# Kernel optimization log

Measured on AMD Instinct MI355X. Metric: run time of the kernel, lower is better.

The kernel has to match this reference:

```python
import jax, jax.numpy as jnp
import numpy as np

D_MODEL = 1024

def setup_inputs() -> dict:
    key = jax.random.key(0)
    ks = jax.random.split(key, 7)
    x = jax.random.normal(ks[0], (4, 2048, D_MODEL), dtype=jnp.float32)
    s = 1.0 / np.sqrt(D_MODEL)
    Wq = jax.random.uniform(ks[1], (D_MODEL, D_MODEL), jnp.float32, -s, s)
    bq = jax.random.uniform(ks[2], (D_MODEL,), jnp.float32, -s, s)
    Wk = jax.random.uniform(ks[3], (D_MODEL, D_MODEL), jnp.float32, -s, s)
    bk = jax.random.uniform(ks[4], (D_MODEL,), jnp.float32, -s, s)
    Wv = jax.random.uniform(ks[5], (D_MODEL, D_MODEL), jnp.float32, -s, s)
    bv = jax.random.uniform(ks[6], (D_MODEL,), jnp.float32, -s, s)
    return {"x": x, "Wq": Wq, "bq": bq, "Wk": Wk, "bk": bk, "Wv": Wv, "bv": bv}

def reference(x, Wq, bq, Wk, bk, Wv, bv):
    # single-head self-attention: q,k,v are [B, S, D]
    q = x @ Wq + bq
    k = x @ Wk + bk
    v = x @ Wv + bv
    scale = 1.0 / jnp.sqrt(jnp.asarray(D_MODEL, x.dtype))
    scores = jnp.einsum('bsd,btd->bst', q, k) * scale  # [B, S, S]
    attn = jax.nn.softmax(scores, axis=-1)
    return jnp.einsum('bst,btd->bsd', attn, v)
```

## Files before the change

kernel.cpp:

```cpp
#include <hip/hip_runtime.h>
#include <hip/hip_bf16.h>
#include <stdint.h>


typedef __attribute__((ext_vector_type(8))) short short8;
typedef __attribute__((ext_vector_type(4))) float f32x4;

__device__ __forceinline__ unsigned short f2bf(float f) {
  union { float f; uint32_t u; } c; c.f = f;
  uint32_t u = c.u;
  u += 0x7FFFu + ((u >> 16) & 1u);
  return (unsigned short)(u >> 16);
}

__device__ __forceinline__ void gl16(const void* g, void* l) {
  __builtin_amdgcn_global_load_lds(
      (const __attribute__((address_space(1))) unsigned int*)g,
      (__attribute__((address_space(3))) unsigned int*)l, 16, 0, 0);
}

template <int MODE>
__device__ __forceinline__ void gemm_body(
    int z, int tm, int tn,
    const short* __restrict__ A, const short* __restrict__ B,
    void* __restrict__ Cv, short* __restrict__ vT, float scale,
    const float* __restrict__ bias0, const float* __restrict__ bias1,
    const float* __restrict__ bias2, float* __restrict__ rowsum)
{
  constexpr int  LDA = (MODE == 2) ? 2048 : 1024;
  constexpr int  LDB = (MODE == 2) ? 2048 : 1024;
  constexpr int  LDC = (MODE == 0) ? 1024 : ((MODE == 1) ? 2048 : 1024);
  constexpr long SAZ = (MODE == 0) ? 0L : ((MODE == 1) ? 2097152L : 4194304L);
  constexpr long SBZ = (MODE == 0) ? 1048576L : 2097152L;
  constexpr long SCZ = (MODE == 0) ? 8388608L : ((MODE == 1) ? 4194304L : 2097152L);
  constexpr int  T   = (MODE == 2) ? 64 : 32;

  __shared__ short lds[18432];

  const int tid  = threadIdx.x;
  const int lane = tid & 63;
  const int wid  = tid >> 6;
  const long tileM = (long)tm * 128;
  const long tileN = (long)tn * 128;
  const short* Az = A + (long)z * SAZ;
  const short* Bz = B + (long)z * SBZ;

  const int c0 = tid, c1 = 256 + tid;
  const short* gA0 = Az + (tileM + (c0 >> 2)) * LDA + (c0 & 3) * 8;
  const short* gA1 = Az + (tileM + (c1 >> 2)) * LDA + (c1 & 3) * 8;
  const short* gB0 = Bz + (tileN + (c0 >> 2)) * LDB + (c0 & 3) * 8;
  const short* gB1 = Bz + (tileN + (c1 >> 2)) * LDB + (c1 & 3) * 8;

  const int fr = lane & 15, quad = lane >> 4;
  const int waveM = (wid >> 1) * 64, waveN = (wid & 1) * 64;

  f32x4 acc[4][4] = {};

  {
    short* base = lds;
    gl16(gA0, base + c0 * 8);
    gl16(gA1, base + c1 * 8);
    gl16(gB0, base + 4096 + c0 * 8);
    gl16(gB1, base + 4096 + c1 * 8);
  }

  for (int t = 0; t < T; ++t) {
    __syncthreads();
    if (t + 1 < T) {
      const int kt = (t + 1) << 5;
      short* base = lds + ((t + 1) & 1) * 8192;
      gl16(gA0 + kt, base + c0 * 8);
      gl16(gA1 + kt, base + c1 * 8);
      gl16(gB0 + kt, base + 4096 + c0 * 8);
      gl16(gB1 + kt, base + 4096 + c1 * 8);
    }
    const short* sA = lds + (t & 1) * 8192;
    const short* sB = sA + 4096;
    short8 af[4], bf[4];
#pragma unroll
    for (int i = 0; i < 4; ++i)
      af[i] = *(const short8*)&sA[(waveM + i * 16 + fr) * 32 + quad * 8];
#pragma unroll
    for (int j = 0; j < 4; ++j)
      bf[j] = *(const short8*)&sB[(waveN + j * 16 + fr) * 32 + quad * 8];
#pragma unroll
    for (int i = 0; i < 4; ++i)
#pragma unroll
      for (int j = 0; j < 4; ++j)
        acc[i][j] = __builtin_amdgcn_mfma_f32_16x16x32_bf16(af[i], bf[j],
                                                            acc[i][j], 0, 0, 0);
  }

  if (MODE == 1) {
#pragma unroll
    for (int i = 0; i < 4; ++i)
#pragma unroll
      for (int j = 0; j < 4; ++j)
#pragma unroll
        for (int r = 0; r < 4; ++r)
          acc[i][j][r] = exp2f(acc[i][j][r] * scale);
#pragma unroll
    for (int i = 0; i < 4; ++i)
#pragma unroll
      for (int r = 0; r < 4; ++r) {
        float s = acc[i][0][r] + acc[i][1][r] + acc[i][2][r] + acc[i][3][r];
        s += __shfl_xor(s, 1);
        s += __shfl_xor(s, 2);
        s += __shfl_xor(s, 4);
        s += __shfl_xor(s, 8);
        if (fr == 0)
          atomicAdd(&rowsum[(long)z * 2048 + tileM + waveM + i * 16 + quad * 4 + r], s);
      }
  }

  if (MODE == 0 && z == 2) {
    __syncthreads();
    short* scr = lds + wid * 4608;
#pragma unroll
    for (int j = 0; j < 4; ++j) {
      const float bv = bias2[tileN + waveN + j * 16 + fr];
#pragma unroll
      for (int i = 0; i < 4; ++i)
#pragma unroll
        for (int r = 0; r < 4; ++r)
          scr[(j * 16 + fr) * 72 + i * 16 + quad * 4 + r] =
              (short)f2bf(acc[i][j][r] + bv);
    }
    const int gb = tm >> 4;
    const long t0 = (long)(tm & 15) * 128 + waveM;
#pragma unroll
    for (int c = 0; c < 8; ++c) {
      const int rr = c * 8 + (lane >> 3);
      const int cc = (lane & 7) * 8;
      short8 v = *(const short8*)&scr[rr * 72 + cc];
      const long gd = tileN + waveN + rr;
      *(short8*)(vT + ((long)gb << 21) + gd * 2048 + t0 + cc) = v;
    }
  } else if (MODE <= 1) {
    __syncthreads();
    short* scr = lds + wid * 4608;
    short* C = (short*)Cv + (long)z * SCZ;
    const float* bias = (z == 0) ? bias0 : bias1;
#pragma unroll
    for (int j = 0; j < 4; ++j) {
      const float bv = (MODE == 0) ? bias[tileN + waveN + j * 16 + fr] : 0.0f;
#pragma unroll
      for (int i = 0; i < 4; ++i)
#pragma unroll
        for (int r = 0; r < 4; ++r)
          scr[(i * 16 + quad * 4 + r) * 72 + j * 16 + fr] =
              (short)f2bf(acc[i][j][r] + bv);
    }
#pragma unroll
    for (int c = 0; c < 8; ++c) {
      const int row = c * 8 + (lane >> 3);
      const int col = (lane & 7) * 8;
      short8 v = *(const short8*)&scr[row * 72 + col];
      *(short8*)(C + (tileM + waveM + row) * LDC + tileN + waveN + col) = v;
    }
  } else {
    float* C = (float*)Cv + (long)z * SCZ;
#pragma unroll
    for (int i = 0; i < 4; ++i)
#pragma unroll
      for (int r = 0; r < 4; ++r) {
        const long gr = tileM + waveM + i * 16 + quad * 4 + r;
        const float rinv = 1.0f / rowsum[(long)z * 2048 + gr];
#pragma unroll
        for (int j = 0; j < 4; ++j)
          C[gr * LDC + tileN + waveN + j * 16 + fr] = acc[i][j][r] * rinv;
      }
  }
}

__global__ __launch_bounds__(256) void k_qkv(
    const short* __restrict__ A, const short* __restrict__ B,
    void* __restrict__ Cv, short* __restrict__ vT,
    const float* __restrict__ b0, const float* __restrict__ b1,
    const float* __restrict__ b2)
{
  gemm_body<0>(blockIdx.z, blockIdx.y, blockIdx.x, A, B, Cv, vT, 1.0f,
               b0, b1, b2, nullptr);
}

__global__ __launch_bounds__(256) void k_score(
    const short* __restrict__ A, const short* __restrict__ B,
    void* __restrict__ Cv, float scale, float* __restrict__ rowsum)
{
  const int b = blockIdx.x;
  const int xcd = b & 7, r = b >> 3;
  const int z = r >> 5;
  const int pair = (r >> 4) & 1, mem = r & 15;
  const int s = pair * 8 + xcd;
  const int tm = (s >> 2) * 4 + (mem >> 2);
  const int tn = (s & 3) * 4 + (mem & 3);
  gemm_body<1>(z, tm, tn, A, B, Cv, nullptr, scale,
               nullptr, nullptr, nullptr, rowsum);
}

__global__ __launch_bounds__(256) void k_pv(
    const short* __restrict__ A, const short* __restrict__ B,
    void* __restrict__ Cv, float* __restrict__ rowsum)
{
  const int b = blockIdx.x;
  const int s = b & 7, r = b >> 3;
  const int z = r >> 4;
  const int mem = r & 15;
  const int tm = (s >> 1) * 4 + (mem >> 2);
  const int tn = (s & 1) * 4 + (mem & 3);
  gemm_body<2>(z, tm, tn, A, B, Cv, nullptr, 1.0f,
               nullptr, nullptr, nullptr, rowsum);
}

__global__ __launch_bounds__(256) void k_prep(
    const float4* __restrict__ x, ushort4* __restrict__ xb,
    const float* __restrict__ Wq, const float* __restrict__ Wk,
    const float* __restrict__ Wv, short* __restrict__ WT,
    float* __restrict__ rs)
{
  __shared__ short tile[32][33];
  const int b = blockIdx.x;
  if (b < 8192) {
    const long i = (long)b * 256 + threadIdx.x;
    float4 v = x[i];
    ushort4 o;
    o.x = f2bf(v.x); o.y = f2bf(v.y); o.z = f2bf(v.z); o.w = f2bf(v.w);
    xb[i] = o;
  } else if (b < 11264) {
    const int idx = b - 8192;
    const int z = idx >> 10, rem = idx & 1023;
    const float* W = (z == 0) ? Wq : ((z == 1) ? Wk : Wv);
    short* d = WT + (long)z * 1024 * 1024;
    const int n0 = (rem & 31) * 32, d0 = (rem >> 5) * 32;
    const int tx = threadIdx.x & 31, ty = threadIdx.x >> 5;
#pragma unroll
    for (int p = 0; p < 4; ++p)
      tile[ty + p * 8][tx] = (short)f2bf(W[(long)(d0 + ty + p * 8) * 1024 + n0 + tx]);
    __syncthreads();
#pragma unroll
    for (int p = 0; p < 4; ++p)
      d[(long)(n0 + ty + p * 8) * 1024 + d0 + tx] = tile[tx][ty + p * 8];
  } else {
#pragma unroll
    for (int p = 0; p < 32; ++p)
      rs[p * 256 + threadIdx.x] = 0.0f;
  }
}

extern "C" void kernel_launch(void* const* d_in, const int* in_sizes, int n_in,
                              void* d_out, int out_size, void* d_ws, size_t ws_size,
                              hipStream_t stream) {
  const float* x  = (const float*)d_in[0];
  const float* Wq = (const float*)d_in[1];
  const float* bq = (const float*)d_in[2];
  const float* Wk = (const float*)d_in[3];
  const float* bk = (const float*)d_in[4];
  const float* Wv = (const float*)d_in[5];
  const float* bv = (const float*)d_in[6];

  char* ws = (char*)d_ws;
  short* xb  = (short*)(ws);
  short* wt  = (short*)(ws + 16777216);
  short* qkv = (short*)(ws + 23068672);
  short* Pp  = (short*)(ws + 73400320);
  float* rs  = (float*)(ws + 106954752);
  short* vT  = qkv + 2L * 8388608;

  k_prep<<<11265, 256, 0, stream>>>((const float4*)x, (ushort4*)xb,
                                    Wq, Wk, Wv, wt, rs);
  k_qkv<<<dim3(8, 64, 3), 256, 0, stream>>>(xb, wt, qkv, vT, bq, bk, bv);
  k_score<<<1024, 256, 0, stream>>>(qkv, qkv + 8388608, Pp,
                                    0.03125f * 1.44269504088896f, rs);
  k_pv<<<512, 256, 0, stream>>>(Pp, vT, d_out, rs);
}
```

Measured before the change: 279.1 us.

## Use 64x128 tiles with 128-thread blocks for score and PV GEMMs

Splits the shared GEMM template so the QKV projection keeps 128x128 tiles, while the score and PV GEMMs use 64x128 tiles with two waves per block. This doubles their grid sizes and changes the tile-to-block mapping, dropping the XCD-aware ordering. The V transpose moves out of the QKV epilogue into a separate LDS-tiled transpose kernel with its own workspace buffer. The smaller tiles aim for better occupancy and load balance, at the cost of less reuse per block, an extra kernel launch and an extra pass over V in global memory.

Result: slower. 313.6 us (+12.3%).

```diff
diff --git a/kernel.cpp b/kernel.cpp
--- a/kernel.cpp
+++ b/kernel.cpp
@@ -19,37 +19,28 @@
       (__attribute__((address_space(3))) unsigned int*)l, 16, 0, 0);
 }
 
-template <int MODE>
-__device__ __forceinline__ void gemm_body(
-    int z, int tm, int tn,
+__global__ __launch_bounds__(256) void k_qkv(
     const short* __restrict__ A, const short* __restrict__ B,
-    void* __restrict__ Cv, short* __restrict__ vT, float scale,
-    const float* __restrict__ bias0, const float* __restrict__ bias1,
-    const float* __restrict__ bias2, float* __restrict__ rowsum)
-{
-  constexpr int  LDA = (MODE == 2) ? 2048 : 1024;
-  constexpr int  LDB = (MODE == 2) ? 2048 : 1024;
-  constexpr int  LDC = (MODE == 0) ? 1024 : ((MODE == 1) ? 2048 : 1024);
-  constexpr long SAZ = (MODE == 0) ? 0L : ((MODE == 1) ? 2097152L : 4194304L);
-  constexpr long SBZ = (MODE == 0) ? 1048576L : 2097152L;
-  constexpr long SCZ = (MODE == 0) ? 8388608L : ((MODE == 1) ? 4194304L : 2097152L);
-  constexpr int  T   = (MODE == 2) ? 64 : 32;
-
+    short* __restrict__ Cb,
+    const float* __restrict__ b0, const float* __restrict__ b1,
+    const float* __restrict__ b2)
+{
   __shared__ short lds[18432];
 
   const int tid  = threadIdx.x;
   const int lane = tid & 63;
   const int wid  = tid >> 6;
-  const long tileM = (long)tm * 128;
-  const long tileN = (long)tn * 128;
-  const short* Az = A + (long)z * SAZ;
-  const short* Bz = B + (long)z * SBZ;
+  const int z    = blockIdx.z;
+  const long tileM = (long)blockIdx.y * 128;
+  const long tileN = (long)blockIdx.x * 128;
+  const short* Az = A;
+  const short* Bz = B + (long)z * 1048576L;
 
   const int c0 = tid, c1 = 256 + tid;
-  const short* gA0 = Az + (tileM + (c0 >> 2)) * LDA + (c0 & 3) * 8;
-  const short* gA1 = Az + (tileM + (c1 >> 2)) * LDA + (c1 & 3) * 8;
-  const short* gB0 = Bz + (tileN + (c0 >> 2)) * LDB + (c0 & 3) * 8;
-  const short* gB1 = Bz + (tileN + (c1 >> 2)) * LDB + (c1 & 3) * 8;
+  const short* gA0 = Az + (tileM + (c0 >> 2)) * 1024 + (c0 & 3) * 8;
+  const short* gA1 = Az + (tileM + (c1 >> 2)) * 1024 + (c1 & 3) * 8;
+  const short* gB0 = Bz + (tileN + (c0 >> 2)) * 1024 + (c0 & 3) * 8;
+  const short* gB1 = Bz + (tileN + (c1 >> 2)) * 1024 + (c1 & 3) * 8;
 
   const int fr = lane & 15, quad = lane >> 4;
   const int waveM = (wid >> 1) * 64, waveN = (wid & 1) * 64;
@@ -64,9 +55,9 @@
     gl16(gB1, base + 4096 + c1 * 8);
   }
 
-  for (int t = 0; t < T; ++t) {
+  for (int t = 0; t < 32; ++t) {
     __syncthreads();
-    if (t + 1 < T) {
+    if (t + 1 < 32) {
       const int kt = (t + 1) << 5;
       short* base = lds + ((t + 1) & 1) * 8192;
       gl16(gA0 + kt, base + c0 * 8);
@@ -91,6 +82,106 @@
                                                             acc[i][j], 0, 0, 0);
   }
 
+  __syncthreads();
+  short* scr = lds + wid * 4608;
+  short* C = Cb + (long)z * 8388608L;
+  const float* bias = (z == 0) ? b0 : ((z == 1) ? b1 : b2);
+#pragma unroll
+  for (int j = 0; j < 4; ++j) {
+    const float bv = bias[tileN + waveN + j * 16 + fr];
+#pragma unroll
+    for (int i = 0; i < 4; ++i)
+#pragma unroll
+      for (int r = 0; r < 4; ++r)
+        scr[(i * 16 + quad * 4 + r) * 72 + j * 16 + fr] =
+            (short)f2bf(acc[i][j][r] + bv);
+  }
+#pragma unroll
+  for (int c = 0; c < 8; ++c) {
+    const int row = c * 8 + (lane >> 3);
+    const int col = (lane & 7) * 8;
+    short8 v = *(const short8*)&scr[row * 72 + col];
+    *(short8*)(C + (tileM + waveM + row) * 1024 + tileN + waveN + col) = v;
+  }
+}
+
+template <int MODE>
+__device__ __forceinline__ void body128(
+    int z, int tm, int tn,
+    const short* __restrict__ A, const short* __restrict__ B,
+    void* __restrict__ Cv, float scale, float* __restrict__ rowsum)
+{
+  constexpr int  LDA = (MODE == 2) ? 2048 : 1024;
+  constexpr int  LDB = (MODE == 2) ? 2048 : 1024;
+  constexpr int  LDC = (MODE == 1) ? 2048 : 1024;
+  constexpr long SAZ = (MODE == 1) ? 2097152L : 4194304L;
+  constexpr long SBZ = 2097152L;
+  constexpr long SCZ = (MODE == 1) ? 4194304L : 2097152L;
+  constexpr int  T   = (MODE == 2) ? 64 : 32;
+
+  __shared__ short lds[12288];
+
+  const int tid  = threadIdx.x;
+  const int lane = tid & 63;
+  const int wid  = tid >> 6;
+  const long tileM = (long)tm * 64;
+  const long tileN = (long)tn * 128;
+  const short* Az = A + (long)z * SAZ;
+  const short* Bz = B + (long)z * SBZ;
+
+  const int cA0 = tid, cA1 = 128 + tid;
+  const short* gA0 = Az + (tileM + (cA0 >> 2)) * LDA + (cA0 & 3) * 8;
+  const short* gA1 = Az + (tileM + (cA1 >> 2)) * LDA + (cA1 & 3) * 8;
+  const int cB0 = tid, cB1 = 128 + tid, cB2 = 256 + tid, cB3 = 384 + tid;
+  const short* gB0 = Bz + (tileN + (cB0 >> 2)) * LDB + (cB0 & 3) * 8;
+  const short* gB1 = Bz + (tileN + (cB1 >> 2)) * LDB + (cB1 & 3) * 8;
+  const short* gB2 = Bz + (tileN + (cB2 >> 2)) * LDB + (cB2 & 3) * 8;
+  const short* gB3 = Bz + (tileN + (cB3 >> 2)) * LDB + (cB3 & 3) * 8;
+
+  const int fr = lane & 15, quad = lane >> 4;
+  const int waveN = wid * 64;
+
+  f32x4 acc[4][4] = {};
+
+  {
+    short* base = lds;
+    gl16(gA0, base + cA0 * 8);
+    gl16(gA1, base + cA1 * 8);
+    gl16(gB0, base + 2048 + cB0 * 8);
+    gl16(gB1, base + 2048 + cB1 * 8);
+    gl16(gB2, base + 2048 + cB2 * 8);
+    gl16(gB3, base + 2048 + cB3 * 8);
+  }
+
+  for (int t = 0; t < T; ++t) {
+    __syncthreads();
+    if (t + 1 < T) {
+      const int kt = (t + 1) << 5;
+      short* base = lds + ((t + 1) & 1) * 6144;
+      gl16(gA0 + kt, base + cA0 * 8);
+      gl16(gA1 + kt, base + cA1 * 8);
+      gl16(gB0 + kt, base + 2048 + cB0 * 8);
+      gl16(gB1 + kt, base + 2048 + cB1 * 8);
+      gl16(gB2 + kt, base + 2048 + cB2 * 8);
+      gl16(gB3 + kt, base + 2048 + cB3 * 8);
+    }
+    const short* sA = lds + (t & 1) * 6144;
+    const short* sB = sA + 2048;
+    short8 af[4], bf[4];
+#pragma unroll
+    for (int i = 0; i < 4; ++i)
+      af[i] = *(const short8*)&sA[(i * 16 + fr) * 32 + quad * 8];
+#pragma unroll
+    for (int j = 0; j < 4; ++j)
+      bf[j] = *(const short8*)&sB[(waveN + j * 16 + fr) * 32 + quad * 8];
+#pragma unroll
+    for (int i = 0; i < 4; ++i)
+#pragma unroll
+      for (int j = 0; j < 4; ++j)
+        acc[i][j] = __builtin_amdgcn_mfma_f32_16x16x32_bf16(af[i], bf[j],
+                                                            acc[i][j], 0, 0, 0);
+  }
+
   if (MODE == 1) {
 #pragma unroll
     for (int i = 0; i < 4; ++i)
@@ -109,54 +200,25 @@
         s += __shfl_xor(s, 4);
         s += __shfl_xor(s, 8);
         if (fr == 0)
-          atomicAdd(&rowsum[(long)z * 2048 + tileM + waveM + i * 16 + quad * 4 + r], s);
+          atomicAdd(&rowsum[(long)z * 2048 + tileM + i * 16 + quad * 4 + r], s);
       }
-  }
-
-  if (MODE == 0 && z == 2) {
-    __syncthreads();
-    short* scr = lds + wid * 4608;
-#pragma unroll
-    for (int j = 0; j < 4; ++j) {
-      const float bv = bias2[tileN + waveN + j * 16 + fr];
-#pragma unroll
-      for (int i = 0; i < 4; ++i)
-#pragma unroll
-        for (int r = 0; r < 4; ++r)
-          scr[(j * 16 + fr) * 72 + i * 16 + quad * 4 + r] =
-              (short)f2bf(acc[i][j][r] + bv);
-    }
-    const int gb = tm >> 4;
-    const long t0 = (long)(tm & 15) * 128 + waveM;
-#pragma unroll
-    for (int c = 0; c < 8; ++c) {
-      const int rr = c * 8 + (lane >> 3);
-      const int cc = (lane & 7) * 8;
-      short8 v = *(const short8*)&scr[rr * 72 + cc];
-      const long gd = tileN + waveN + rr;
-      *(short8*)(vT + ((long)gb << 21) + gd * 2048 + t0 + cc) = v;
-    }
-  } else if (MODE <= 1) {
     __syncthreads();
     short* scr = lds + wid * 4608;
     short* C = (short*)Cv + (long)z * SCZ;
-    const float* bias = (z == 0) ? bias0 : bias1;
-#pragma unroll
-    for (int j = 0; j < 4; ++j) {
-      const float bv = (MODE == 0) ? bias[tileN + waveN + j * 16 + fr] : 0.0f;
+#pragma unroll
+    for (int j = 0; j < 4; ++j)
 #pragma unroll
       for (int i = 0; i < 4; ++i)
 #pragma unroll
         for (int r = 0; r < 4; ++r)
           scr[(i * 16 + quad * 4 + r) * 72 + j * 16 + fr] =
-              (short)f2bf(acc[i][j][r] + bv);
-    }
+              (short)f2bf(acc[i][j][r]);
 #pragma unroll
     for (int c = 0; c < 8; ++c) {
       const int row = c * 8 + (lane >> 3);
       const int col = (lane & 7) * 8;
       short8 v = *(const short8*)&scr[row * 72 + col];
-      *(short8*)(C + (tileM + waveM + row) * LDC + tileN + waveN + col) = v;
+      *(short8*)(C + (tileM + row) * LDC + tileN + waveN + col) = v;
     }
   } else {
     float* C = (float*)Cv + (long)z * SCZ;
@@ -164,7 +226,7 @@
     for (int i = 0; i < 4; ++i)
 #pragma unroll
       for (int r = 0; r < 4; ++r) {
-        const long gr = tileM + waveM + i * 16 + quad * 4 + r;
+        const long gr = tileM + i * 16 + quad * 4 + r;
         const float rinv = 1.0f / rowsum[(long)z * 2048 + gr];
 #pragma unroll
         for (int j = 0; j < 4; ++j)
@@ -173,43 +235,46 @@
   }
 }
 
-__global__ __launch_bounds__(256) void k_qkv(
-    const short* __restrict__ A, const short* __restrict__ B,
-    void* __restrict__ Cv, short* __restrict__ vT,
-    const float* __restrict__ b0, const float* __restrict__ b1,
-    const float* __restrict__ b2)
-{
-  gemm_body<0>(blockIdx.z, blockIdx.y, blockIdx.x, A, B, Cv, vT, 1.0f,
-               b0, b1, b2, nullptr);
-}
-
-__global__ __launch_bounds__(256) void k_score(
+__global__ __launch_bounds__(128) void k_score(
     const short* __restrict__ A, const short* __restrict__ B,
     void* __restrict__ Cv, float scale, float* __restrict__ rowsum)
 {
   const int b = blockIdx.x;
-  const int xcd = b & 7, r = b >> 3;
-  const int z = r >> 5;
-  const int pair = (r >> 4) & 1, mem = r & 15;
-  const int s = pair * 8 + xcd;
-  const int tm = (s >> 2) * 4 + (mem >> 2);
-  const int tn = (s & 3) * 4 + (mem & 3);
-  gemm_body<1>(z, tm, tn, A, B, Cv, nullptr, scale,
-               nullptr, nullptr, nullptr, rowsum);
-}
-
-__global__ __launch_bounds__(256) void k_pv(
+  const int z = b >> 9, rest = b & 511;
+  const int super = rest >> 4, inner = rest & 15;
+  const int tm = (super >> 2) * 4 + (inner >> 2);
+  const int tn = (super & 3) * 4 + (inner & 3);
+  body128<1>(z, tm, tn, A, B, Cv, scale, rowsum);
+}
+
+__global__ __launch_bounds__(128) void k_pv(
     const short* __restrict__ A, const short* __restrict__ B,
     void* __restrict__ Cv, float* __restrict__ rowsum)
 {
   const int b = blockIdx.x;
-  const int s = b & 7, r = b >> 3;
-  const int z = r >> 4;
-  const int mem = r & 15;
-  const int tm = (s >> 1) * 4 + (mem >> 2);
-  const int tn = (s & 1) * 4 + (mem & 3);
-  gemm_body<2>(z, tm, tn, A, B, Cv, nullptr, 1.0f,
-               nullptr, nullptr, nullptr, rowsum);
+  const int z = b >> 8, rest = b & 255;
+  const int super = rest >> 4, inner = rest & 15;
+  const int tm = (super >> 1) * 4 + (inner >> 2);
+  const int tn = (super & 1) * 4 + (inner & 3);
+  body128<2>(z, tm, tn, A, B, Cv, 1.0f, rowsum);
+}
+
+__global__ __launch_bounds__(256) void k_tr(
+    const short* __restrict__ src, short* __restrict__ dst)
+{
+  __shared__ short tile[32][33];
+  const int z = blockIdx.z;
+  const int d0 = blockIdx.x * 32, t0 = blockIdx.y * 32;
+  const int tx = threadIdx.x & 31, ty = threadIdx.x >> 5;
+  const short* s = src + (long)z * 2048 * 1024;
+  short* d = dst + (long)z * 1024 * 2048;
+#pragma unroll
+  for (int p = 0; p < 4; ++p)
+    tile[ty + p * 8][tx] = s[(long)(t0 + ty + p * 8) * 1024 + d0 + tx];
+  __syncthreads();
+#pragma unroll
+  for (int p = 0; p < 4; ++p)
+    d[(long)(d0 + ty + p * 8) * 2048 + t0 + tx] = tile[tx][ty + p * 8];
 }
 
 __global__ __launch_bounds__(256) void k_prep(
@@ -264,12 +329,13 @@
   short* qkv = (short*)(ws + 23068672);
   short* Pp  = (short*)(ws + 73400320);
   float* rs  = (float*)(ws + 106954752);
-  short* vT  = qkv + 2L * 8388608;
+  short* vT  = (short*)(ws + 106987520);
 
   k_prep<<<11265, 256, 0, stream>>>((const float4*)x, (ushort4*)xb,
                                     Wq, Wk, Wv, wt, rs);
-  k_qkv<<<dim3(8, 64, 3), 256, 0, stream>>>(xb, wt, qkv, vT, bq, bk, bv);
-  k_score<<<1024, 256, 0, stream>>>(qkv, qkv + 8388608, Pp,
+  k_qkv<<<dim3(8, 64, 3), 256, 0, stream>>>(xb, wt, qkv, bq, bk, bv);
+  k_tr<<<dim3(32, 64, 4), 256, 0, stream>>>(qkv + 2L * 8388608, vT);
+  k_score<<<2048, 128, 0, stream>>>(qkv, qkv + 8388608, Pp,
                                     0.03125f * 1.44269504088896f, rs);
-  k_pv<<<512, 256, 0, stream>>>(Pp, vT, d_out, rs);
-}
+  k_pv<<<1024, 128, 0, stream>>>(Pp, vT, d_out, rs);
+}
```

## Use 256x256 tiles with 1024-thread blocks for scores and XCD-aware QKV grid mapping

Applied to the files above, without the earlier changes.

The templated GEMM body is split into three specialized kernels. The score GEMM now uses 256x256 output tiles with 16 waves per 1024-thread block, and each block loads the whole K tile for the larger tile. That raises operand reuse and halves global loads per output element. The QKV kernel gets a 1D grid remapped so that the M-tiles sharing one XCD are grouped together, aiming at better L2 locality. The trade-off is larger LDS use, lower occupancy, and a serialized four-round epilogue for writing the score tiles.

Result: faster. 256.2 us (-8.2%).

```diff
diff --git a/kernel.cpp b/kernel.cpp
--- a/kernel.cpp
+++ b/kernel.cpp
@@ -19,21 +19,18 @@
       (__attribute__((address_space(3))) unsigned int*)l, 16, 0, 0);
 }
 
-template <int MODE>
-__device__ __forceinline__ void gemm_body(
-    int z, int tm, int tn,
+__global__ __launch_bounds__(256) void k_qkv(
     const short* __restrict__ A, const short* __restrict__ B,
-    void* __restrict__ Cv, short* __restrict__ vT, float scale,
-    const float* __restrict__ bias0, const float* __restrict__ bias1,
-    const float* __restrict__ bias2, float* __restrict__ rowsum)
+    short* __restrict__ Cb, short* __restrict__ vT,
+    const float* __restrict__ b0, const float* __restrict__ b1,
+    const float* __restrict__ b2)
 {
-  constexpr int  LDA = (MODE == 2) ? 2048 : 1024;
-  constexpr int  LDB = (MODE == 2) ? 2048 : 1024;
-  constexpr int  LDC = (MODE == 0) ? 1024 : ((MODE == 1) ? 2048 : 1024);
-  constexpr long SAZ = (MODE == 0) ? 0L : ((MODE == 1) ? 2097152L : 4194304L);
-  constexpr long SBZ = (MODE == 0) ? 1048576L : 2097152L;
-  constexpr long SCZ = (MODE == 0) ? 8388608L : ((MODE == 1) ? 4194304L : 2097152L);
-  constexpr int  T   = (MODE == 2) ? 64 : 32;
+  const int b = blockIdx.x;
+  const int xcd = b & 7, r = b >> 3;
+  const int z = r >> 6;
+  const int mem = r & 63;
+  const int tm = xcd * 8 + (mem >> 3);
+  const int tn = mem & 7;
 
   __shared__ short lds[18432];
 
@@ -42,14 +39,14 @@
   const int wid  = tid >> 6;
   const long tileM = (long)tm * 128;
   const long tileN = (long)tn * 128;
-  const short* Az = A + (long)z * SAZ;
-  const short* Bz = B + (long)z * SBZ;
+  const short* Az = A;
+  const short* Bz = B + (long)z * 1048576L;
 
   const int c0 = tid, c1 = 256 + tid;
-  const short* gA0 = Az + (tileM + (c0 >> 2)) * LDA + (c0 & 3) * 8;
-  const short* gA1 = Az + (tileM + (c1 >> 2)) * LDA + (c1 & 3) * 8;
-  const short* gB0 = Bz + (tileN + (c0 >> 2)) * LDB + (c0 & 3) * 8;
-  const short* gB1 = Bz + (tileN + (c1 >> 2)) * LDB + (c1 & 3) * 8;
+  const short* gA0 = Az + (tileM + (c0 >> 2)) * 1024 + (c0 & 3) * 8;
+  const short* gA1 = Az + (tileM + (c1 >> 2)) * 1024 + (c1 & 3) * 8;
+  const short* gB0 = Bz + (tileN + (c0 >> 2)) * 1024 + (c0 & 3) * 8;
+  const short* gB1 = Bz + (tileN + (c1 >> 2)) * 1024 + (c1 & 3) * 8;
 
   const int fr = lane & 15, quad = lane >> 4;
   const int waveM = (wid >> 1) * 64, waveN = (wid & 1) * 64;
@@ -64,9 +61,9 @@
     gl16(gB1, base + 4096 + c1 * 8);
   }
 
-  for (int t = 0; t < T; ++t) {
-    __syncthreads();
-    if (t + 1 < T) {
+  for (int t = 0; t < 32; ++t) {
+    __syncthreads();
+    if (t + 1 < 32) {
       const int kt = (t + 1) << 5;
       short* base = lds + ((t + 1) & 1) * 8192;
       gl16(gA0 + kt, base + c0 * 8);
@@ -91,34 +88,12 @@
                                                             acc[i][j], 0, 0, 0);
   }
 
-  if (MODE == 1) {
-#pragma unroll
-    for (int i = 0; i < 4; ++i)
-#pragma unroll
-      for (int j = 0; j < 4; ++j)
-#pragma unroll
-        for (int r = 0; r < 4; ++r)
-          acc[i][j][r] = exp2f(acc[i][j][r] * scale);
-#pragma unroll
-    for (int i = 0; i < 4; ++i)
-#pragma unroll
-      for (int r = 0; r < 4; ++r) {
-        float s = acc[i][0][r] + acc[i][1][r] + acc[i][2][r] + acc[i][3][r];
-        s += __shfl_xor(s, 1);
-        s += __shfl_xor(s, 2);
-        s += __shfl_xor(s, 4);
-        s += __shfl_xor(s, 8);
-        if (fr == 0)
-          atomicAdd(&rowsum[(long)z * 2048 + tileM + waveM + i * 16 + quad * 4 + r], s);
-      }
-  }
-
-  if (MODE == 0 && z == 2) {
+  if (z == 2) {
     __syncthreads();
     short* scr = lds + wid * 4608;
 #pragma unroll
     for (int j = 0; j < 4; ++j) {
-      const float bv = bias2[tileN + waveN + j * 16 + fr];
+      const float bv = b2[tileN + waveN + j * 16 + fr];
 #pragma unroll
       for (int i = 0; i < 4; ++i)
 #pragma unroll
@@ -136,14 +111,14 @@
       const long gd = tileN + waveN + rr;
       *(short8*)(vT + ((long)gb << 21) + gd * 2048 + t0 + cc) = v;
     }
-  } else if (MODE <= 1) {
+  } else {
     __syncthreads();
     short* scr = lds + wid * 4608;
-    short* C = (short*)Cv + (long)z * SCZ;
-    const float* bias = (z == 0) ? bias0 : bias1;
+    short* C = Cb + (long)z * 8388608L;
+    const float* bias = (z == 0) ? b0 : b1;
 #pragma unroll
     for (int j = 0; j < 4; ++j) {
-      const float bv = (MODE == 0) ? bias[tileN + waveN + j * 16 + fr] : 0.0f;
+      const float bv = bias[tileN + waveN + j * 16 + fr];
 #pragma unroll
       for (int i = 0; i < 4; ++i)
 #pragma unroll
@@ -156,60 +131,191 @@
       const int row = c * 8 + (lane >> 3);
       const int col = (lane & 7) * 8;
       short8 v = *(const short8*)&scr[row * 72 + col];
-      *(short8*)(C + (tileM + waveM + row) * LDC + tileN + waveN + col) = v;
-    }
-  } else {
-    float* C = (float*)Cv + (long)z * SCZ;
-#pragma unroll
-    for (int i = 0; i < 4; ++i)
-#pragma unroll
-      for (int r = 0; r < 4; ++r) {
-        const long gr = tileM + waveM + i * 16 + quad * 4 + r;
-        const float rinv = 1.0f / rowsum[(long)z * 2048 + gr];
-#pragma unroll
-        for (int j = 0; j < 4; ++j)
-          C[gr * LDC + tileN + waveN + j * 16 + fr] = acc[i][j][r] * rinv;
-      }
-  }
-}
-
-__global__ __launch_bounds__(256) void k_qkv(
+      *(short8*)(C + (tileM + waveM + row) * 1024 + tileN + waveN + col) = v;
+    }
+  }
+}
+
+__global__ __launch_bounds__(1024) void k_score(
     const short* __restrict__ A, const short* __restrict__ B,
-    void* __restrict__ Cv, short* __restrict__ vT,
-    const float* __restrict__ b0, const float* __restrict__ b1,
-    const float* __restrict__ b2)
-{
-  gemm_body<0>(blockIdx.z, blockIdx.y, blockIdx.x, A, B, Cv, vT, 1.0f,
-               b0, b1, b2, nullptr);
-}
-
-__global__ __launch_bounds__(256) void k_score(
-    const short* __restrict__ A, const short* __restrict__ B,
-    void* __restrict__ Cv, float scale, float* __restrict__ rowsum)
+    short* __restrict__ Pp, float scale, float* __restrict__ rowsum)
 {
   const int b = blockIdx.x;
-  const int xcd = b & 7, r = b >> 3;
-  const int z = r >> 5;
-  const int pair = (r >> 4) & 1, mem = r & 15;
-  const int s = pair * 8 + xcd;
-  const int tm = (s >> 2) * 4 + (mem >> 2);
-  const int tn = (s & 3) * 4 + (mem & 3);
-  gemm_body<1>(z, tm, tn, A, B, Cv, nullptr, scale,
-               nullptr, nullptr, nullptr, rowsum);
+  const int z = b >> 6;
+  const int tm = (b & 63) >> 3, tn = b & 7;
+
+  __shared__ short lds[32768];
+
+  const int tid  = threadIdx.x;
+  const int lane = tid & 63;
+  const int wid  = tid >> 6;
+  const long tileM = (long)tm * 256;
+  const long tileN = (long)tn * 256;
+  const short* Az = A + (long)z * 2097152L;
+  const short* Bz = B + (long)z * 2097152L;
+
+  const short* gA = Az + (tileM + (tid >> 2)) * 1024 + (tid & 3) * 8;
+  const short* gB = Bz + (tileN + (tid >> 2)) * 1024 + (tid & 3) * 8;
+
+  const int fr = lane & 15, quad = lane >> 4;
+  const int waveM = (wid >> 2) * 64, waveN = (wid & 3) * 64;
+
+  f32x4 acc[4][4] = {};
+
+  {
+    short* base = lds;
+    gl16(gA, base + tid * 8);
+    gl16(gB, base + 8192 + tid * 8);
+  }
+
+  for (int t = 0; t < 32; ++t) {
+    __syncthreads();
+    if (t + 1 < 32) {
+      const int kt = (t + 1) << 5;
+      short* base = lds + ((t + 1) & 1) * 16384;
+      gl16(gA + kt, base + tid * 8);
+      gl16(gB + kt, base + 8192 + tid * 8);
+    }
+    const short* sA = lds + (t & 1) * 16384;
+    const short* sB = sA + 8192;
+    short8 af[4], bf[4];
+#pragma unroll
+    for (int i = 0; i < 4; ++i)
+      af[i] = *(const short8*)&sA[(waveM + i * 16 + fr) * 32 + quad * 8];
+#pragma unroll
+    for (int j = 0; j < 4; ++j)
+      bf[j] = *(const short8*)&sB[(waveN + j * 16 + fr) * 32 + quad * 8];
+#pragma unroll
+    for (int i = 0; i < 4; ++i)
+#pragma unroll
+      for (int j = 0; j < 4; ++j)
+        acc[i][j] = __builtin_amdgcn_mfma_f32_16x16x32_bf16(af[i], bf[j],
+                                                            acc[i][j], 0, 0, 0);
+  }
+
+#pragma unroll
+  for (int i = 0; i < 4; ++i)
+#pragma unroll
+    for (int j = 0; j < 4; ++j)
+#pragma unroll
+      for (int r = 0; r < 4; ++r)
+        acc[i][j][r] = exp2f(acc[i][j][r] * scale);
+#pragma unroll
+  for (int i = 0; i < 4; ++i)
+#pragma unroll
+    for (int r = 0; r < 4; ++r) {
+      float s = acc[i][0][r] + acc[i][1][r] + acc[i][2][r] + acc[i][3][r];
+      s += __shfl_xor(s, 1);
+      s += __shfl_xor(s, 2);
+      s += __shfl_xor(s, 4);
+      s += __shfl_xor(s, 8);
+      if (fr == 0)
+        atomicAdd(&rowsum[(long)z * 2048 + tileM + waveM + i * 16 + quad * 4 + r], s);
+    }
+
+  short* C = Pp + (long)z * 4194304L;
+  const int wgrp = wid >> 2, wloc = wid & 3;
+  for (int rnd = 0; rnd < 4; ++rnd) {
+    __syncthreads();
+    if (wgrp == rnd) {
+      short* scr = lds + wloc * 4608;
+#pragma unroll
+      for (int j = 0; j < 4; ++j)
+#pragma unroll
+        for (int i = 0; i < 4; ++i)
+#pragma unroll
+          for (int r = 0; r < 4; ++r)
+            scr[(i * 16 + quad * 4 + r) * 72 + j * 16 + fr] =
+                (short)f2bf(acc[i][j][r]);
+#pragma unroll
+      for (int c = 0; c < 8; ++c) {
+        const int row = c * 8 + (lane >> 3);
+        const int col = (lane & 7) * 8;
+        short8 v = *(const short8*)&scr[row * 72 + col];
+        *(short8*)(C + (tileM + waveM + row) * 2048 + tileN + waveN + col) = v;
+      }
+    }
+  }
 }
 
 __global__ __launch_bounds__(256) void k_pv(
     const short* __restrict__ A, const short* __restrict__ B,
-    void* __restrict__ Cv, float* __restrict__ rowsum)
+    float* __restrict__ Cf, float* __restrict__ rowsum)
 {
   const int b = blockIdx.x;
-  const int s = b & 7, r = b >> 3;
-  const int z = r >> 4;
-  const int mem = r & 15;
+  const int s = b & 7, r0_ = b >> 3;
+  const int z = r0_ >> 4;
+  const int mem = r0_ & 15;
   const int tm = (s >> 1) * 4 + (mem >> 2);
   const int tn = (s & 1) * 4 + (mem & 3);
-  gemm_body<2>(z, tm, tn, A, B, Cv, nullptr, 1.0f,
-               nullptr, nullptr, nullptr, rowsum);
+
+  __shared__ short lds[18432];
+
+  const int tid  = threadIdx.x;
+  const int lane = tid & 63;
+  const int wid  = tid >> 6;
+  const long tileM = (long)tm * 128;
+  const long tileN = (long)tn * 128;
+  const short* Az = A + (long)z * 4194304L;
+  const short* Bz = B + (long)z * 2097152L;
+
+  const int c0 = tid, c1 = 256 + tid;
+  const short* gA0 = Az + (tileM + (c0 >> 2)) * 2048 + (c0 & 3) * 8;
+  const short* gA1 = Az + (tileM + (c1 >> 2)) * 2048 + (c1 & 3) * 8;
+  const short* gB0 = Bz + (tileN + (c0 >> 2)) * 2048 + (c0 & 3) * 8;
+  const short* gB1 = Bz + (tileN + (c1 >> 2)) * 2048 + (c1 & 3) * 8;
+
+  const int fr = lane & 15, quad = lane >> 4;
+  const int waveM = (wid >> 1) * 64, waveN = (wid & 1) * 64;
+
+  f32x4 acc[4][4] = {};
+
+  {
+    short* base = lds;
+    gl16(gA0, base + c0 * 8);
+    gl16(gA1, base + c1 * 8);
+    gl16(gB0, base + 4096 + c0 * 8);
+    gl16(gB1, base + 4096 + c1 * 8);
+  }
+
+  for (int t = 0; t < 64; ++t) {
+    __syncthreads();
+    if (t + 1 < 64) {
+      const int kt = (t + 1) << 5;
+      short* base = lds + ((t + 1) & 1) * 8192;
+      gl16(gA0 + kt, base + c0 * 8);
+      gl16(gA1 + kt, base + c1 * 8);
+      gl16(gB0 + kt, base + 4096 + c0 * 8);
+      gl16(gB1 + kt, base + 4096 + c1 * 8);
+    }
+    const short* sA = lds + (t & 1) * 8192;
+    const short* sB = sA + 4096;
+    short8 af[4], bf[4];
+#pragma unroll
+    for (int i = 0; i < 4; ++i)
+      af[i] = *(const short8*)&sA[(waveM + i * 16 + fr) * 32 + quad * 8];
+#pragma unroll
+    for (int j = 0; j < 4; ++j)
+      bf[j] = *(const short8*)&sB[(waveN + j * 16 + fr) * 32 + quad * 8];
+#pragma unroll
+    for (int i = 0; i < 4; ++i)
+#pragma unroll
+      for (int j = 0; j < 4; ++j)
+        acc[i][j] = __builtin_amdgcn_mfma_f32_16x16x32_bf16(af[i], bf[j],
+                                                            acc[i][j], 0, 0, 0);
+  }
+
+  float* C = Cf + (long)z * 2097152L;
+#pragma unroll
+  for (int i = 0; i < 4; ++i)
+#pragma unroll
+    for (int r = 0; r < 4; ++r) {
+      const long gr = tileM + waveM + i * 16 + quad * 4 + r;
+      const float rinv = 1.0f / rowsum[(long)z * 2048 + gr];
+#pragma unroll
+      for (int j = 0; j < 4; ++j)
+        C[gr * 1024 + tileN + waveN + j * 16 + fr] = acc[i][j][r] * rinv;
+    }
 }
 
 __global__ __launch_bounds__(256) void k_prep(
@@ -268,8 +374,8 @@
 
   k_prep<<<11265, 256, 0, stream>>>((const float4*)x, (ushort4*)xb,
                                     Wq, Wk, Wv, wt, rs);
-  k_qkv<<<dim3(8, 64, 3), 256, 0, stream>>>(xb, wt, qkv, vT, bq, bk, bv);
-  k_score<<<1024, 256, 0, stream>>>(qkv, qkv + 8388608, Pp,
+  k_qkv<<<1536, 256, 0, stream>>>(xb, wt, qkv, vT, bq, bk, bv);
+  k_score<<<256, 1024, 0, stream>>>(qkv, qkv + 8388608, Pp,
                                     0.03125f * 1.44269504088896f, rs);
-  k_pv<<<512, 256, 0, stream>>>(Pp, vT, d_out, rs);
-}
+  k_pv<<<512, 256, 0, stream>>>(Pp, vT, (float*)d_out, rs);
+}
```
